# Performance work log

Measured on AMD Instinct MI355X. Metric: run time of the kernel, lower is better.

## Reference

```python
import jax, jax.numpy as jnp
import numpy as np
from jax import lax

WORD_NUM = 30000
EMBED = 128
RNN = 256
CLASSES = 9
BATCH = 128
SEQ = 512


def setup_inputs() -> dict:
    key = jax.random.key(0)
    ks = jax.random.split(key, 7)
    s_e = 1.0 / np.sqrt(EMBED)
    s_r = 1.0 / np.sqrt(RNN)
    return {
        "input_x": jax.random.randint(ks[0], (BATCH, SEQ), 0, WORD_NUM, dtype=jnp.int32),
        "embed": jax.random.normal(ks[1], (WORD_NUM, EMBED), dtype=jnp.float32) * 0.05,
        # LSTM kernel/recurrent kernel, gate order i|f|g|o (Keras convention)
        "W": jax.random.normal(ks[2], (EMBED, 4 * RNN), dtype=jnp.float32) * s_e,
        "U": jax.random.normal(ks[3], (RNN, 4 * RNN), dtype=jnp.float32) * s_r,
        "b": jnp.zeros((4 * RNN,), dtype=jnp.float32),
        "Wout": jax.random.normal(ks[4], (RNN, CLASSES), dtype=jnp.float32) * s_r,
        "bout": jnp.zeros((CLASSES,), dtype=jnp.float32),
    }


def _lstm(xs, W, U, b, h0, c0):
    # xs: [T, B, E] -> hidden sequence [T, B, R], final (h, c)
    def step(carry, x):
        h, c = carry
        z = x @ W + h @ U + b  # [B, 4R]
        i, f, g, o = jnp.split(z, 4, axis=-1)
        i = jax.nn.sigmoid(i)
        f = jax.nn.sigmoid(f)
        g = jnp.tanh(g)
        o = jax.nn.sigmoid(o)
        c = f * c + i * g
        h = o * jnp.tanh(c)
        return (h, c), h

    (h, c), hs = lax.scan(step, (h0, c0), xs)
    return hs, h, c


def reference(input_x, embed, W, U, b, Wout, bout):
    # Embedding lookup: [B, S] -> [B, S, E]
    x = embed[input_x]
    B = x.shape[0]
    R = U.shape[0]
    h0 = jnp.zeros((B, R), dtype=x.dtype)
    c0 = jnp.zeros((B, R), dtype=x.dtype)
    xs = jnp.swapaxes(x, 0, 1)  # [S, B, E] for time-major scan
    hs, h_last, c_last = _lstm(xs, W, U, b, h0, c0)
    hs = jnp.swapaxes(hs, 0, 1)  # [B, S, R]
    probs = jax.nn.softmax(hs @ Wout + bout, axis=-1)  # [B, S, C]
    # Keras return_state -> (sequence_output, last_h, last_c); state=(hc, hs)
    return probs, (h_last, c_last)
```

## Files before the change

kernel.cpp:

```cpp
#include <hip/hip_runtime.h>
#include <math.h>

#define B 128
#define S 512
#define E 128
#define R 256
#define G4 1024

static const size_t HS_FLOATS = 513ull * (R / 4) * (B * 4);
static const size_t X4_OFF    = HS_FLOATS;
static const size_t WUT_OFF   = X4_OFF + (size_t)S * (E / 4) * (B * 4);
static const size_t SYNC_OFF  = WUT_OFF + (size_t)G4 * 384;
static const size_t WS_FLOATS = SYNC_OFF + 1024;

#define HOUT_OFF 589824
#define COUT_OFF 622592

__global__ void zero_state(float* __restrict__ HS, int* __restrict__ sync) {
    int i = blockIdx.x * 1024 + threadIdx.x;
    if (i < 32768) HS[i] = 0.f;
    if (i < 1024) sync[i] = 0;
}

__global__ void gather_x(const int* __restrict__ idx, const float* __restrict__ embed,
                         float4* __restrict__ X4) {
    int t    = blockIdx.x;
    int tid  = threadIdx.x;
    int b    = tid & 127;
    int half = tid >> 7;
    int row  = idx[(size_t)b * S + t];
    const float4* er = (const float4*)embed + (size_t)row * (E / 4);
    size_t xbase = (size_t)t * (E / 4) * B + b;
#pragma unroll
    for (int kk = 0; kk < 16; ++kk) {
        int e4 = half * 16 + kk;
        X4[xbase + (size_t)e4 * B] = er[e4];
    }
}

__global__ void make_wut(const float* __restrict__ W, const float* __restrict__ U,
                         float* __restrict__ WUt) {
    int j = blockIdx.x;
    int s = threadIdx.x;
    float v = (s < E) ? W[(size_t)s * G4 + j] : U[(size_t)(s - E) * G4 + j];
    WUt[(size_t)j * 384 + s] = v;
}

__device__ __forceinline__ float sigmoidf_(float x) { return 1.f / (1.f + __expf(-x)); }

__launch_bounds__(512, 2)
__global__ void lstm_persist(const float4* __restrict__ X4, const float* __restrict__ WUt,
                             const float* __restrict__ bias, float* __restrict__ HS,
                             float* __restrict__ out, int* __restrict__ sync) {
    const int tid  = threadIdx.x;
    const int lane = tid & 63;
    const int wid  = __builtin_amdgcn_readfirstlane((int)(tid >> 6));
    const int k    = wid & 3;
    const int rl   = wid >> 2;
    const int w    = blockIdx.x;
    const int rpair = w >> 1;
    const int bg    = w & 1;
    const int r     = rpair * 2 + rl;
    const int b     = bg * 64 + lane;
    const int xg    = w & 7;

    __shared__ float partial[2][3][4][64];

    const float* wu0 = WUt + (size_t)(0 * R + r) * 384;
    const float* wu1 = WUt + (size_t)(1 * R + r) * 384;
    const float* wu2 = WUt + (size_t)(2 * R + r) * 384;
    const float* wu3 = WUt + (size_t)(3 * R + r) * 384;

    int* cnt1 = sync + xg * 64;
    int* flg1 = sync + 512 + xg * 64;
    int* cntr = sync + 1016;
    int* flgr = sync + 1020;

    float c = 0.f;

    for (int t = 0; t < S; ++t) {
        float a0, a1, a2, a3;
        if (k == 0) { a0 = bias[r]; a1 = bias[R + r]; a2 = bias[2 * R + r]; a3 = bias[3 * R + r]; }
        else        { a0 = a1 = a2 = a3 = 0.f; }

        const float4* xp = X4 + (size_t)t * (E / 4) * B;
        const float4* hp = (const float4*)HS + (size_t)t * (R / 4) * B;

#define MACX(E0, E1)                                                                   \
        _Pragma("unroll")                                                              \
        for (int m = (E0); m < (E1); ++m) {                                            \
            float4 v = xp[(size_t)m * B + b];                                          \
            int s = m * 4;                                                             \
            a0 += wu0[s] * v.x; a0 += wu0[s+1] * v.y; a0 += wu0[s+2] * v.z; a0 += wu0[s+3] * v.w; \
            a1 += wu1[s] * v.x; a1 += wu1[s+1] * v.y; a1 += wu1[s+2] * v.z; a1 += wu1[s+3] * v.w; \
            a2 += wu2[s] * v.x; a2 += wu2[s+1] * v.y; a2 += wu2[s+2] * v.z; a2 += wu2[s+3] * v.w; \
            a3 += wu3[s] * v.x; a3 += wu3[s+1] * v.y; a3 += wu3[s+2] * v.z; a3 += wu3[s+3] * v.w; \
        }
#define MACH(R0, R1)                                                                   \
        _Pragma("unroll")                                                              \
        for (int m = (R0); m < (R1); ++m) {                                            \
            float4 v = hp[(size_t)m * B + b];                                          \
            int s = E + m * 4;                                                         \
            a0 += wu0[s] * v.x; a0 += wu0[s+1] * v.y; a0 += wu0[s+2] * v.z; a0 += wu0[s+3] * v.w; \
            a1 += wu1[s] * v.x; a1 += wu1[s+1] * v.y; a1 += wu1[s+2] * v.z; a1 += wu1[s+3] * v.w; \
            a2 += wu2[s] * v.x; a2 += wu2[s+1] * v.y; a2 += wu2[s+2] * v.z; a2 += wu2[s+3] * v.w; \
            a3 += wu3[s] * v.x; a3 += wu3[s+1] * v.y; a3 += wu3[s+2] * v.z; a3 += wu3[s+3] * v.w; \
        }

        if (k == 0)      { MACX(0, 24) }
        else if (k == 1) { MACX(24, 32) MACH(0, 16) }
        else if (k == 2) { MACH(16, 40) }
        else             { MACH(40, 64) }
#undef MACX
#undef MACH

        if (k != 0) {
            partial[rl][k - 1][0][lane] = a0;
            partial[rl][k - 1][1][lane] = a1;
            partial[rl][k - 1][2][lane] = a2;
            partial[rl][k - 1][3][lane] = a3;
        }
        __syncthreads();

        if (k == 0) {
#pragma unroll
            for (int kk = 0; kk < 3; ++kk) {
                a0 += partial[rl][kk][0][lane];
                a1 += partial[rl][kk][1][lane];
                a2 += partial[rl][kk][2][lane];
                a3 += partial[rl][kk][3][lane];
            }
            float ig = sigmoidf_(a0);
            float fg = sigmoidf_(a1);
            float gg = tanhf(a2);
            float og = sigmoidf_(a3);
            c = fg * c + ig * gg;
            float h = og * tanhf(c);
            float* haddr = HS + ((size_t)(t + 1) * (R / 4) + (r >> 2)) * (B * 4) + (size_t)b * 4 + (r & 3);
            asm volatile("global_store_dword %0, %1, off sc0 sc1" :: "v"(haddr), "v"(h) : "memory");
            if (t == S - 1) {
                out[HOUT_OFF + (size_t)b * R + r] = h;
                out[COUT_OFF + (size_t)b * R + r] = c;
            }
        }
        asm volatile("s_waitcnt vmcnt(0)" ::: "memory");
        __syncthreads();

        if (t < S - 1) {
            if (tid == 0) {
                int epoch = t + 1;
                int a = __hip_atomic_fetch_add(cnt1, 1, __ATOMIC_ACQ_REL, __HIP_MEMORY_SCOPE_AGENT);
                if (a == 31) {
                    __hip_atomic_store(cnt1, 0, __ATOMIC_RELAXED, __HIP_MEMORY_SCOPE_AGENT);
                    int rr = __hip_atomic_fetch_add(cntr, 1, __ATOMIC_ACQ_REL, __HIP_MEMORY_SCOPE_AGENT);
                    if (rr == 7) {
                        __hip_atomic_store(cntr, 0, __ATOMIC_RELAXED, __HIP_MEMORY_SCOPE_AGENT);
                        __hip_atomic_store(flgr, epoch, __ATOMIC_RELEASE, __HIP_MEMORY_SCOPE_AGENT);
                    } else {
                        int it = 0;
                        while (__hip_atomic_load(flgr, __ATOMIC_RELAXED, __HIP_MEMORY_SCOPE_AGENT) < epoch
                               && ++it < (1 << 20)) __builtin_amdgcn_s_sleep(2);
                    }
                    __hip_atomic_store(flg1, epoch, __ATOMIC_RELEASE, __HIP_MEMORY_SCOPE_AGENT);
                } else {
                    int it = 0;
                    while (__hip_atomic_load(flg1, __ATOMIC_RELAXED, __HIP_MEMORY_SCOPE_AGENT) < epoch
                           && ++it < (1 << 20)) __builtin_amdgcn_s_sleep(2);
                }
            }
            __syncthreads();
        }
    }
}

__global__ void out_probs(const float* __restrict__ HS, const float* __restrict__ Wout,
                          const float* __restrict__ bout, float* __restrict__ out) {
    int t    = blockIdx.x;
    int bg   = blockIdx.y;
    int lane = threadIdx.x;
    int b    = bg * 64 + lane;
    float acc[9];
#pragma unroll
    for (int c = 0; c < 9; ++c) acc[c] = bout[c];
    const float4* hp = (const float4*)HS + (size_t)(t + 1) * (R / 4) * B + b;
#pragma unroll 4
    for (int r4 = 0; r4 < R / 4; ++r4) {
        float4 hv = hp[(size_t)r4 * B];
        int r = r4 * 4;
#pragma unroll
        for (int c = 0; c < 9; ++c) {
            acc[c] += hv.x * Wout[(size_t)(r + 0) * 9 + c];
            acc[c] += hv.y * Wout[(size_t)(r + 1) * 9 + c];
            acc[c] += hv.z * Wout[(size_t)(r + 2) * 9 + c];
            acc[c] += hv.w * Wout[(size_t)(r + 3) * 9 + c];
        }
    }
    float m = acc[0];
#pragma unroll
    for (int c = 1; c < 9; ++c) m = fmaxf(m, acc[c]);
    float e[9];
    float sum = 0.f;
#pragma unroll
    for (int c = 0; c < 9; ++c) { e[c] = expf(acc[c] - m); sum += e[c]; }
    float inv = 1.f / sum;
#pragma unroll
    for (int c = 0; c < 9; ++c) out[((size_t)b * S + t) * 9 + c] = e[c] * inv;
}

extern "C" void kernel_launch(void* const* d_in, const int* in_sizes, int n_in,
                              void* d_out, int out_size, void* d_ws, size_t ws_size,
                              hipStream_t stream) {
    const int*   idx   = (const int*)d_in[0];
    const float* embed = (const float*)d_in[1];
    const float* W     = (const float*)d_in[2];
    const float* U     = (const float*)d_in[3];
    const float* bias  = (const float*)d_in[4];
    const float* Wout  = (const float*)d_in[5];
    const float* bout  = (const float*)d_in[6];
    float*       out   = (float*)d_out;
    float*       ws    = (float*)d_ws;

    if (ws_size < WS_FLOATS * sizeof(float)) return;

    float*  HS   = ws;
    float4* X4   = (float4*)(ws + X4_OFF);
    float*  WUt  = ws + WUT_OFF;
    int*    sync = (int*)(ws + SYNC_OFF);

    zero_state<<<32, 1024, 0, stream>>>(HS, sync);
    gather_x<<<S, 256, 0, stream>>>(idx, embed, X4);
    make_wut<<<G4, 384, 0, stream>>>(W, U, WUt);
    lstm_persist<<<256, 512, 0, stream>>>(X4, WUt, bias, HS, out, sync);
    out_probs<<<dim3(S, 2), 64, 0, stream>>>(HS, Wout, bout, out);
}
```

Before: 4.741 ms.

## Partition LSTM by batch groups with register-resident weights and local group sync

The persistent LSTM kernel is restructured so each workgroup handles 4 batch rows and 32 hidden units across all four gates. Its weight slice stays in registers, and the x and h activations are staged in LDS. Synchronisation now happens only among the 8 workgroups that share a batch group, replacing the two-level barrier across all workgroups, and h is double-buffered in a small ping-pong array. The output projection and softmax are fused into the recurrent loop, with workgroups taking turns per step, and the kernel is launched cooperatively. This cuts the global barrier latency and repeated weight loads per step, at the cost of heavy register pressure and an extra LDS staging round trip.

```diff
diff --git a/kernel.cpp b/kernel.cpp
--- a/kernel.cpp
+++ b/kernel.cpp
@@ -5,206 +5,223 @@
 #define S 512
 #define E 128
 #define R 256
-#define G4 1024
-
-static const size_t HS_FLOATS = 513ull * (R / 4) * (B * 4);
-static const size_t X4_OFF    = HS_FLOATS;
-static const size_t WUT_OFF   = X4_OFF + (size_t)S * (E / 4) * (B * 4);
-static const size_t SYNC_OFF  = WUT_OFF + (size_t)G4 * 384;
+
+#define NG 32
+#define QW 8
+#define ELS 4
+#define OUTS 128
+#define UNITS 32
+
+typedef float v2f __attribute__((ext_vector_type(2)));
+
+static const size_t HX_OFF   = 0;
+static const size_t XG_OFF   = HX_OFF + 2ull * B * R;
+static const size_t WUT_OFF  = XG_OFF + (size_t)S * B * E;
+static const size_t SYNC_OFF = WUT_OFF + 1024ull * 384;
 static const size_t WS_FLOATS = SYNC_OFF + 1024;
 
 #define HOUT_OFF 589824
 #define COUT_OFF 622592
 
-__global__ void zero_state(float* __restrict__ HS, int* __restrict__ sync) {
-    int i = blockIdx.x * 1024 + threadIdx.x;
-    if (i < 32768) HS[i] = 0.f;
-    if (i < 1024) sync[i] = 0;
+__global__ void zero_sync(int* __restrict__ sync) {
+    sync[threadIdx.x] = 0;
 }
 
 __global__ void gather_x(const int* __restrict__ idx, const float* __restrict__ embed,
-                         float4* __restrict__ X4) {
+                         float* __restrict__ Xg) {
     int t    = blockIdx.x;
     int tid  = threadIdx.x;
-    int b    = tid & 127;
-    int half = tid >> 7;
+    int b    = tid >> 1;
+    int half = tid & 1;
     int row  = idx[(size_t)b * S + t];
-    const float4* er = (const float4*)embed + (size_t)row * (E / 4);
-    size_t xbase = (size_t)t * (E / 4) * B + b;
-#pragma unroll
-    for (int kk = 0; kk < 16; ++kk) {
-        int e4 = half * 16 + kk;
-        X4[xbase + (size_t)e4 * B] = er[e4];
-    }
+    const float4* er = (const float4*)(embed + (size_t)row * E) + half * 16;
+    float4* xw = (float4*)(Xg + ((size_t)t * B + b) * E) + half * 16;
+#pragma unroll
+    for (int k = 0; k < 16; ++k) xw[k] = er[k];
 }
 
 __global__ void make_wut(const float* __restrict__ W, const float* __restrict__ U,
                          float* __restrict__ WUt) {
     int j = blockIdx.x;
     int s = threadIdx.x;
-    float v = (s < E) ? W[(size_t)s * G4 + j] : U[(size_t)(s - E) * G4 + j];
+    float v = (s < E) ? W[(size_t)s * 1024 + j] : U[(size_t)(s - E) * 1024 + j];
     WUt[(size_t)j * 384 + s] = v;
 }
 
-__device__ __forceinline__ float sigmoidf_(float x) { return 1.f / (1.f + __expf(-x)); }
+__device__ __forceinline__ float sigm(float x) { return 1.f / (1.f + __expf(-x)); }
 
 __launch_bounds__(512, 2)
-__global__ void lstm_persist(const float4* __restrict__ X4, const float* __restrict__ WUt,
-                             const float* __restrict__ bias, float* __restrict__ HS,
-                             float* __restrict__ out, int* __restrict__ sync) {
+__global__ void lstm_persist(const float* __restrict__ Xg, const float* __restrict__ WUt,
+                             const float* __restrict__ bias, const float* __restrict__ Wout,
+                             const float* __restrict__ bout, float* __restrict__ out,
+                             float* __restrict__ HX, int* __restrict__ sync) {
+    __shared__ float act[ELS][E + R];
+    __shared__ float partial[4][ELS][OUTS];
+    __shared__ float woutT[9][260];
+    __shared__ float zrow[ELS][12];
+
     const int tid  = threadIdx.x;
+    const int wg   = blockIdx.x;
+    const int g    = wg >> 3;
+    const int q    = wg & 7;
     const int lane = tid & 63;
-    const int wid  = __builtin_amdgcn_readfirstlane((int)(tid >> 6));
-    const int k    = wid & 3;
-    const int rl   = wid >> 2;
-    const int w    = blockIdx.x;
-    const int rpair = w >> 1;
-    const int bg    = w & 1;
-    const int r     = rpair * 2 + rl;
-    const int b     = bg * 64 + lane;
-    const int xg    = w & 7;
-
-    __shared__ float partial[2][3][4][64];
-
-    const float* wu0 = WUt + (size_t)(0 * R + r) * 384;
-    const float* wu1 = WUt + (size_t)(1 * R + r) * 384;
-    const float* wu2 = WUt + (size_t)(2 * R + r) * 384;
-    const float* wu3 = WUt + (size_t)(3 * R + r) * 384;
-
-    int* cnt1 = sync + xg * 64;
-    int* flg1 = sync + 512 + xg * 64;
-    int* cntr = sync + 1016;
-    int* flgr = sync + 1020;
-
-    float c = 0.f;
+    const int wv   = __builtin_amdgcn_readfirstlane(tid >> 6);
+    const int ks   = wv >> 1;
+    const int oi   = ((wv & 1) << 6) | lane;
+    const int j    = (oi >> 5) * 256 + q * 32 + (oi & 31);
+
+    float4 wx[8], wh[16];
+    {
+        const float4* wrow = (const float4*)(WUt + (size_t)j * 384);
+#pragma unroll
+        for (int p = 0; p < 8; ++p)  wx[p] = wrow[8 * ks + p];
+#pragma unroll
+        for (int p = 0; p < 16; ++p) wh[p] = wrow[32 + 16 * ks + p];
+    }
+
+    float bias_g0 = 0.f, bias_g1 = 0.f, bias_g2 = 0.f, bias_g3 = 0.f, creg = 0.f;
+    if (tid < 128) {
+        int u = tid & 31;
+        bias_g0 = bias[0 * 256 + q * 32 + u];
+        bias_g1 = bias[1 * 256 + q * 32 + u];
+        bias_g2 = bias[2 * 256 + q * 32 + u];
+        bias_g3 = bias[3 * 256 + q * 32 + u];
+    }
+    float boutr = 0.f;
+    if (wv == 0 && (lane & 15) < 9) boutr = bout[lane & 15];
+
+    for (int i = tid; i < 9 * 256; i += 512) {
+        int c = i >> 8, r = i & 255;
+        woutT[c][r] = Wout[(size_t)r * 9 + c];
+    }
+    for (int i = tid; i < ELS * (E + R); i += 512) ((float*)act)[i] = 0.f;
+    __syncthreads();
+    if (tid < 256) {
+        int el = tid >> 6, e2 = (tid & 63) * 2;
+        *(v2f*)&act[el][e2] = *(const v2f*)&Xg[((size_t)0 * B + g * 4 + el) * E + e2];
+    }
+    __syncthreads();
+
+    int* cnt = sync + g * 32;
+    int* flg = sync + g * 32 + 16;
 
     for (int t = 0; t < S; ++t) {
-        float a0, a1, a2, a3;
-        if (k == 0) { a0 = bias[r]; a1 = bias[R + r]; a2 = bias[2 * R + r]; a3 = bias[3 * R + r]; }
-        else        { a0 = a1 = a2 = a3 = 0.f; }
-
-        const float4* xp = X4 + (size_t)t * (E / 4) * B;
-        const float4* hp = (const float4*)HS + (size_t)t * (R / 4) * B;
-
-#define MACX(E0, E1)                                                                   \
-        _Pragma("unroll")                                                              \
-        for (int m = (E0); m < (E1); ++m) {                                            \
-            float4 v = xp[(size_t)m * B + b];                                          \
-            int s = m * 4;                                                             \
-            a0 += wu0[s] * v.x; a0 += wu0[s+1] * v.y; a0 += wu0[s+2] * v.z; a0 += wu0[s+3] * v.w; \
-            a1 += wu1[s] * v.x; a1 += wu1[s+1] * v.y; a1 += wu1[s+2] * v.z; a1 += wu1[s+3] * v.w; \
-            a2 += wu2[s] * v.x; a2 += wu2[s+1] * v.y; a2 += wu2[s+2] * v.z; a2 += wu2[s+3] * v.w; \
-            a3 += wu3[s] * v.x; a3 += wu3[s+1] * v.y; a3 += wu3[s+2] * v.z; a3 += wu3[s+3] * v.w; \
-        }
-#define MACH(R0, R1)                                                                   \
-        _Pragma("unroll")                                                              \
-        for (int m = (R0); m < (R1); ++m) {                                            \
-            float4 v = hp[(size_t)m * B + b];                                          \
-            int s = E + m * 4;                                                         \
-            a0 += wu0[s] * v.x; a0 += wu0[s+1] * v.y; a0 += wu0[s+2] * v.z; a0 += wu0[s+3] * v.w; \
-            a1 += wu1[s] * v.x; a1 += wu1[s+1] * v.y; a1 += wu1[s+2] * v.z; a1 += wu1[s+3] * v.w; \
-            a2 += wu2[s] * v.x; a2 += wu2[s+1] * v.y; a2 += wu2[s+2] * v.z; a2 += wu2[s+3] * v.w; \
-            a3 += wu3[s] * v.x; a3 += wu3[s+1] * v.y; a3 += wu3[s+2] * v.z; a3 += wu3[s+3] * v.w; \
-        }
-
-        if (k == 0)      { MACX(0, 24) }
-        else if (k == 1) { MACX(24, 32) MACH(0, 16) }
-        else if (k == 2) { MACH(16, 40) }
-        else             { MACH(40, 64) }
-#undef MACX
-#undef MACH
-
-        if (k != 0) {
-            partial[rl][k - 1][0][lane] = a0;
-            partial[rl][k - 1][1][lane] = a1;
-            partial[rl][k - 1][2][lane] = a2;
-            partial[rl][k - 1][3][lane] = a3;
-        }
-        __syncthreads();
-
-        if (k == 0) {
-#pragma unroll
-            for (int kk = 0; kk < 3; ++kk) {
-                a0 += partial[rl][kk][0][lane];
-                a1 += partial[rl][kk][1][lane];
-                a2 += partial[rl][kk][2][lane];
-                a3 += partial[rl][kk][3][lane];
-            }
-            float ig = sigmoidf_(a0);
-            float fg = sigmoidf_(a1);
-            float gg = tanhf(a2);
-            float og = sigmoidf_(a3);
-            c = fg * c + ig * gg;
-            float h = og * tanhf(c);
-            float* haddr = HS + ((size_t)(t + 1) * (R / 4) + (r >> 2)) * (B * 4) + (size_t)b * 4 + (r & 3);
+        float ac0 = 0.f, ac1 = 0.f, ac2 = 0.f, ac3 = 0.f;
+        {
+            const int xo = 32 * ks;
+#pragma unroll
+            for (int p = 0; p < 8; ++p) {
+                float4 w  = wx[p];
+                float4 a0 = *(const float4*)&act[0][xo + 4 * p];
+                float4 a1 = *(const float4*)&act[1][xo + 4 * p];
+                float4 a2 = *(const float4*)&act[2][xo + 4 * p];
+                float4 a3 = *(const float4*)&act[3][xo + 4 * p];
+                ac0 += w.x * a0.x + w.y * a0.y + w.z * a0.z + w.w * a0.w;
+                ac1 += w.x * a1.x + w.y * a1.y + w.z * a1.z + w.w * a1.w;
+                ac2 += w.x * a2.x + w.y * a2.y + w.z * a2.z + w.w * a2.w;
+                ac3 += w.x * a3.x + w.y * a3.y + w.z * a3.z + w.w * a3.w;
+            }
+            const int ho = E + 64 * ks;
+#pragma unroll
+            for (int p = 0; p < 16; ++p) {
+                float4 w  = wh[p];
+                float4 a0 = *(const float4*)&act[0][ho + 4 * p];
+                float4 a1 = *(const float4*)&act[1][ho + 4 * p];
+                float4 a2 = *(const float4*)&act[2][ho + 4 * p];
+                float4 a3 = *(const float4*)&act[3][ho + 4 * p];
+                ac0 += w.x * a0.x + w.y * a0.y + w.z * a0.z + w.w * a0.w;
+                ac1 += w.x * a1.x + w.y * a1.y + w.z * a1.z + w.w * a1.w;
+                ac2 += w.x * a2.x + w.y * a2.y + w.z * a2.z + w.w * a2.w;
+                ac3 += w.x * a3.x + w.y * a3.y + w.z * a3.z + w.w * a3.w;
+            }
+        }
+        partial[ks][0][oi] = ac0;
+        partial[ks][1][oi] = ac1;
+        partial[ks][2][oi] = ac2;
+        partial[ks][3][oi] = ac3;
+        __syncthreads();
+
+        if (tid < 128) {
+            int el = tid >> 5, u = tid & 31;
+            float z0 = bias_g0, z1 = bias_g1, z2 = bias_g2, z3 = bias_g3;
+#pragma unroll
+            for (int kk = 0; kk < 4; ++kk) {
+                z0 += partial[kk][el][0 * 32 + u];
+                z1 += partial[kk][el][1 * 32 + u];
+                z2 += partial[kk][el][2 * 32 + u];
+                z3 += partial[kk][el][3 * 32 + u];
+            }
+            float ig = sigm(z0), fg = sigm(z1), gv = tanhf(z2), og = sigm(z3);
+            creg = fg * creg + ig * gv;
+            float h = og * tanhf(creg);
+            float* haddr = HX + ((size_t)(t & 1) * B + g * 4 + el) * R + q * 32 + u;
             asm volatile("global_store_dword %0, %1, off sc0 sc1" :: "v"(haddr), "v"(h) : "memory");
             if (t == S - 1) {
-                out[HOUT_OFF + (size_t)b * R + r] = h;
-                out[COUT_OFF + (size_t)b * R + r] = c;
-            }
+                out[HOUT_OFF + (size_t)(g * 4 + el) * R + q * 32 + u] = h;
+                out[COUT_OFF + (size_t)(g * 4 + el) * R + q * 32 + u] = creg;
+            }
+        }
+        v2f xpre;
+        const bool do_x = (tid < 256) && (t < S - 1);
+        if (do_x) {
+            int el = tid >> 6, e2 = (tid & 63) * 2;
+            xpre = *(const v2f*)&Xg[((size_t)(t + 1) * B + g * 4 + el) * E + e2];
         }
         asm volatile("s_waitcnt vmcnt(0)" ::: "memory");
         __syncthreads();
 
-        if (t < S - 1) {
-            if (tid == 0) {
-                int epoch = t + 1;
-                int a = __hip_atomic_fetch_add(cnt1, 1, __ATOMIC_ACQ_REL, __HIP_MEMORY_SCOPE_AGENT);
-                if (a == 31) {
-                    __hip_atomic_store(cnt1, 0, __ATOMIC_RELAXED, __HIP_MEMORY_SCOPE_AGENT);
-                    int rr = __hip_atomic_fetch_add(cntr, 1, __ATOMIC_ACQ_REL, __HIP_MEMORY_SCOPE_AGENT);
-                    if (rr == 7) {
-                        __hip_atomic_store(cntr, 0, __ATOMIC_RELAXED, __HIP_MEMORY_SCOPE_AGENT);
-                        __hip_atomic_store(flgr, epoch, __ATOMIC_RELEASE, __HIP_MEMORY_SCOPE_AGENT);
-                    } else {
-                        int it = 0;
-                        while (__hip_atomic_load(flgr, __ATOMIC_RELAXED, __HIP_MEMORY_SCOPE_AGENT) < epoch
-                               && ++it < (1 << 20)) __builtin_amdgcn_s_sleep(2);
-                    }
-                    __hip_atomic_store(flg1, epoch, __ATOMIC_RELEASE, __HIP_MEMORY_SCOPE_AGENT);
-                } else {
-                    int it = 0;
-                    while (__hip_atomic_load(flg1, __ATOMIC_RELAXED, __HIP_MEMORY_SCOPE_AGENT) < epoch
-                           && ++it < (1 << 20)) __builtin_amdgcn_s_sleep(2);
+        if (tid == 0) {
+            int epoch = t + 1;
+            int old = __hip_atomic_fetch_add(cnt, 1, __ATOMIC_ACQ_REL, __HIP_MEMORY_SCOPE_AGENT);
+            if (old == QW - 1) {
+                __hip_atomic_store(cnt, 0, __ATOMIC_RELAXED, __HIP_MEMORY_SCOPE_AGENT);
+                __hip_atomic_store(flg, epoch, __ATOMIC_RELEASE, __HIP_MEMORY_SCOPE_AGENT);
+            } else {
+                int it = 0;
+                while (__hip_atomic_load(flg, __ATOMIC_RELAXED, __HIP_MEMORY_SCOPE_AGENT) < epoch
+                       && ++it < (1 << 16)) {}
+            }
+        }
+        __syncthreads();
+
+        {
+            int el = tid >> 7, r2 = (tid & 127) * 2;
+            const float* hsrc = HX + ((size_t)(t & 1) * B + g * 4 + el) * R + r2;
+            v2f hv;
+            asm volatile("global_load_dwordx2 %0, %1, off sc0 sc1" : "=v"(hv) : "v"(hsrc) : "memory");
+            asm volatile("s_waitcnt vmcnt(0)" ::: "memory");
+            *(v2f*)&act[el][E + r2] = hv;
+        }
+        if (do_x) {
+            int el = tid >> 6, e2 = (tid & 63) * 2;
+            *(v2f*)&act[el][e2] = xpre;
+        }
+        __syncthreads();
+
+        if (q == (t & 7) && wv == 0) {
+            int el = lane >> 4, c = lane & 15;
+            float z = boutr;
+            if (c < 9) {
+#pragma unroll 16
+                for (int p = 0; p < 64; ++p) {
+                    float4 w = *(const float4*)&woutT[c][4 * p];
+                    float4 a = *(const float4*)&act[el][E + 4 * p];
+                    z += w.x * a.x + w.y * a.y + w.z * a.z + w.w * a.w;
                 }
-            }
-            __syncthreads();
-        }
-    }
-}
-
-__global__ void out_probs(const float* __restrict__ HS, const float* __restrict__ Wout,
-                          const float* __restrict__ bout, float* __restrict__ out) {
-    int t    = blockIdx.x;
-    int bg   = blockIdx.y;
-    int lane = threadIdx.x;
-    int b    = bg * 64 + lane;
-    float acc[9];
-#pragma unroll
-    for (int c = 0; c < 9; ++c) acc[c] = bout[c];
-    const float4* hp = (const float4*)HS + (size_t)(t + 1) * (R / 4) * B + b;
-#pragma unroll 4
-    for (int r4 = 0; r4 < R / 4; ++r4) {
-        float4 hv = hp[(size_t)r4 * B];
-        int r = r4 * 4;
-#pragma unroll
-        for (int c = 0; c < 9; ++c) {
-            acc[c] += hv.x * Wout[(size_t)(r + 0) * 9 + c];
-            acc[c] += hv.y * Wout[(size_t)(r + 1) * 9 + c];
-            acc[c] += hv.z * Wout[(size_t)(r + 2) * 9 + c];
-            acc[c] += hv.w * Wout[(size_t)(r + 3) * 9 + c];
-        }
-    }
-    float m = acc[0];
-#pragma unroll
-    for (int c = 1; c < 9; ++c) m = fmaxf(m, acc[c]);
-    float e[9];
-    float sum = 0.f;
-#pragma unroll
-    for (int c = 0; c < 9; ++c) { e[c] = expf(acc[c] - m); sum += e[c]; }
-    float inv = 1.f / sum;
-#pragma unroll
-    for (int c = 0; c < 9; ++c) out[((size_t)b * S + t) * 9 + c] = e[c] * inv;
+                zrow[el][c] = z;
+            }
+            asm volatile("s_waitcnt lgkmcnt(0)" ::: "memory");
+            if (c < 9) {
+                float m = zrow[el][0];
+#pragma unroll
+                for (int cc = 1; cc < 9; ++cc) m = fmaxf(m, zrow[el][cc]);
+                float ssum = 0.f;
+#pragma unroll
+                for (int cc = 0; cc < 9; ++cc) ssum += __expf(zrow[el][cc] - m);
+                out[((size_t)(g * 4 + el) * S + t) * 9 + c] = __expf(z - m) / ssum;
+            }
+        }
+    }
 }
 
 extern "C" void kernel_launch(void* const* d_in, const int* in_sizes, int n_in,
@@ -217,19 +234,21 @@
     const float* bias  = (const float*)d_in[4];
     const float* Wout  = (const float*)d_in[5];
     const float* bout  = (const float*)d_in[6];
-    float*       out   = (float*)d_out;
+    float*       outp  = (float*)d_out;
     float*       ws    = (float*)d_ws;
 
     if (ws_size < WS_FLOATS * sizeof(float)) return;
 
-    float*  HS   = ws;
-    float4* X4   = (float4*)(ws + X4_OFF);
-    float*  WUt  = ws + WUT_OFF;
-    int*    sync = (int*)(ws + SYNC_OFF);
-
-    zero_state<<<32, 1024, 0, stream>>>(HS, sync);
-    gather_x<<<S, 256, 0, stream>>>(idx, embed, X4);
-    make_wut<<<G4, 384, 0, stream>>>(W, U, WUt);
-    lstm_persist<<<256, 512, 0, stream>>>(X4, WUt, bias, HS, out, sync);
-    out_probs<<<dim3(S, 2), 64, 0, stream>>>(HS, Wout, bout, out);
-}
+    float* HX   = ws + HX_OFF;
+    float* Xg   = ws + XG_OFF;
+    float* WUt  = ws + WUT_OFF;
+    int*   sy   = (int*)(ws + SYNC_OFF);
+
+    zero_sync<<<1, 1024, 0, stream>>>(sy);
+    gather_x<<<S, 256, 0, stream>>>(idx, embed, Xg);
+    make_wut<<<1024, 384, 0, stream>>>(W, U, WUt);
+
+    void* args[] = {&Xg, &WUt, &bias, &Wout, &bout, &outp, &HX, &sy};
+    (void)hipLaunchCooperativeKernel((const void*)lstm_persist, dim3(256), dim3(512),
+                                     args, 0, stream);
+}
```

Result: faster. 4.639 ms (-2.2%).
